# Optimization experiments

Measured on AMD Instinct MI355X. Metric: run time of the kernel, lower is better.

The kernel has to match this reference:

```python
import jax, jax.numpy as jnp
import numpy as np

MARGIN = 0.1
SCALE_POS = 2.0
SCALE_NEG = 50.0
THRESH = 0.5
EPS = 1e-5


def setup_inputs() -> dict:
    key = jax.random.key(0)
    k1, k2 = jax.random.split(key)
    feats = jax.random.normal(k1, (4096, 2, 192), dtype=jnp.float32)
    labels = jax.random.randint(k2, (4096,), 0, 4096, dtype=jnp.int64)
    return {"feats": feats, "labels": labels}


def reference(feats, labels):
    B, n_utt, D = feats.shape
    lab = jnp.repeat(labels, n_utt)            # [N]
    f = feats.reshape(-1, D)                   # [N, D]
    N = f.shape[0]

    sim = f @ f.T                              # [N, N]
    # F.normalize(sim): L2-normalize each row, eps=1e-12
    row_norm = jnp.maximum(jnp.linalg.norm(sim, axis=1, keepdims=True), 1e-12)
    S = sim / row_norm

    same = lab[None, :] == lab[:, None]        # [N, N]
    pos_mask = same & (S < 1.0 - EPS)          # pos_pair_ (includes self if < 1-eps)
    neg_mask = ~same                           # neg_pair_

    min_pos = jnp.min(jnp.where(pos_mask, S, jnp.inf), axis=1)    # per-row min(pos_pair_)
    max_neg = jnp.max(jnp.where(neg_mask, S, -jnp.inf), axis=1)   # per-row max(neg_pair_)

    neg_keep = neg_mask & (S > (min_pos - MARGIN)[:, None])
    pos_keep = pos_mask & (S < (max_neg + MARGIN)[:, None])

    has_neg = jnp.any(neg_keep, axis=1)
    has_pos = jnp.any(pos_keep, axis=1)
    valid = has_neg & has_pos

    pos_sum = jnp.sum(jnp.where(pos_keep, jnp.exp(-SCALE_POS * (S - THRESH)), 0.0), axis=1)
    neg_sum = jnp.sum(jnp.where(neg_keep, jnp.exp(SCALE_NEG * (S - THRESH)), 0.0), axis=1)

    row_loss = (1.0 / SCALE_POS) * jnp.log1p(pos_sum) + (1.0 / SCALE_NEG) * jnp.log1p(neg_sum)
    loss = jnp.sum(jnp.where(valid, row_loss, 0.0)) / N

    # prec1 = percent of rows skipped for having no surviving negatives
    prec1 = jnp.sum(~has_neg).astype(jnp.float32) * 100.0 / N
    return loss, prec1
```

## Files before the change

kernel.cpp:

```cpp
#include <hip/hip_runtime.h>
#include <math.h>

typedef float  f32x4  __attribute__((ext_vector_type(4)));
typedef int    int4v  __attribute__((ext_vector_type(4)));
typedef int    int8v  __attribute__((ext_vector_type(8)));

constexpr float MARGIN    = 0.1f;
constexpr float SCALE_POS = 2.0f;
constexpr float SCALE_NEG = 50.0f;
constexpr float THRESH    = 0.5f;
constexpr float ONE_EPS   = 1.0f - 1e-5f;
constexpr float LOG2E     = 1.4426950408889634f;
constexpr float BC        = -(SCALE_NEG * THRESH * LOG2E);
constexpr float VCUT_COEF = (36.0674f - 30.0f) / (SCALE_NEG * LOG2E);

constexpr int D      = 192;
constexpr int KP     = 256;
constexpr int RT     = 4;
constexpr int RPW    = 64;
constexpr int RPB    = 256;
constexpr int CSPLIT = 32;

constexpr int TILE_B8 = 4096;
constexpr int SCALE1  = 0x7f7f7f7f;

__device__ inline float fast_exp2(float x) {
#if __has_builtin(__builtin_amdgcn_exp2f)
  return __builtin_amdgcn_exp2f(x);
#else
  return exp2f(x);
#endif
}

__device__ inline void pin_frag8(int8v& v) {
  asm volatile("" : "+v"(v));
}

__global__ __launch_bounds__(1024) void k_prep(
    const float* __restrict__ f, unsigned char* __restrict__ pk8, int nrows,
    const int* __restrict__ labs, int* __restrict__ hist_g, int* __restrict__ offs_g,
    int* __restrict__ bucket, float* __restrict__ accum, int n)
{
  if (blockIdx.x < 64) {
    int gid = blockIdx.x * 1024 + threadIdx.x;
    int r = gid >> 3, j = gid & 7;
    if (r >= nrows) return;
    float x[32];
    if (j < 6) {
      const float* src = f + (size_t)r * D + j * 32;
#pragma unroll
      for (int i = 0; i < 8; ++i) {
        float4 v = *(const float4*)(src + i * 4);
        x[i * 4 + 0] = v.x; x[i * 4 + 1] = v.y; x[i * 4 + 2] = v.z; x[i * 4 + 3] = v.w;
      }
    } else {
#pragma unroll
      for (int i = 0; i < 32; ++i) x[i] = 0.f;
    }
    union { int s[8]; int8v v; } u;
#pragma unroll
    for (int i = 0; i < 8; ++i) {
      int p = __builtin_amdgcn_cvt_pk_fp8_f32(x[i * 4 + 0], x[i * 4 + 1], 0, false);
      p     = __builtin_amdgcn_cvt_pk_fp8_f32(x[i * 4 + 2], x[i * 4 + 3], p, true);
      u.s[i] = p;
    }
    int tile = r >> 4, c = r & 15, g = j >> 2, qq = j & 3;
    *(int8v*)(pk8 + (size_t)tile * TILE_B8 + g * 2048 + (qq * 16 + c) * 32) = u.v;
    return;
  }

  __shared__ int histL[4096];
  __shared__ int offsL[4096];
  __shared__ int scanb[1024];
  const int t = threadIdx.x;

  if (t < 3) accum[t] = 0.f;
  for (int i = t; i < 4096; i += 1024) histL[i] = 0;
  __syncthreads();
  for (int i = t; i < n; i += 1024) atomicAdd(&histL[labs[i]], 1);
  __syncthreads();
  int base = t * 4;
  int v[4]; int ls = 0;
  for (int k = 0; k < 4; ++k) { v[k] = ls; ls += histL[base + k]; }
  scanb[t] = ls;
  __syncthreads();
  for (int o = 1; o < 1024; o <<= 1) {
    int x = (t >= o) ? scanb[t - o] : 0;
    __syncthreads();
    scanb[t] += x;
    __syncthreads();
  }
  int ebase = scanb[t] - ls;
  for (int k = 0; k < 4; ++k) {
    offsL[base + k] = ebase + v[k];
    offs_g[base + k] = ebase + v[k];
    hist_g[base + k] = histL[base + k];
  }
  __syncthreads();
  for (int i = t; i < 4096; i += 1024) histL[i] = 0;
  __syncthreads();
  for (int i = t; i < n; i += 1024) {
    int lab = labs[i];
    int p = atomicAdd(&histL[lab], 1);
    bucket[offsL[lab] + p] = i;
  }
}

__global__ __launch_bounds__(256, 2) void k_pass1(
    const unsigned char* __restrict__ pk8, const int* __restrict__ labs,
    float* __restrict__ sumsqP, float* __restrict__ maxnegP,
    int N, int cps)
{
  __shared__ int ldsLab[512];

  const int tid  = threadIdx.x;
  const int lane = tid & 63;
  const int w    = tid >> 6;
  const int q    = lane >> 4;
  const int c    = lane & 15;
  const int cs   = blockIdx.x & (CSPLIT - 1);
  const int rbb  = blockIdx.x / CSPLIT;
  const int rowbase = rbb * RPB + w * RPW;
  const int col0 = cs * cps;
  const int ctile0 = col0 >> 4;
  const int ntiles = cps >> 4;

  for (int i = tid; i < cps; i += 256) ldsLab[i] = labs[(col0 + i) >> 1];

  int8v afr[RT][2];
#pragma unroll
  for (int rt = 0; rt < RT; ++rt)
#pragma unroll
    for (int g = 0; g < 2; ++g) {
      afr[rt][g] = *(const int8v*)(pk8 + (size_t)((rowbase >> 4) + rt) * TILE_B8 + g * 2048 + lane * 32);
      pin_frag8(afr[rt][g]);
    }

  int labrow[RT][4];
#pragma unroll
  for (int rt = 0; rt < RT; ++rt)
#pragma unroll
    for (int rr = 0; rr < 4; ++rr)
      labrow[rt][rr] = labs[(rowbase + rt * 16 + q * 4 + rr) >> 1];

  float ssq[RT][4], mxn[RT][4];
#pragma unroll
  for (int rt = 0; rt < RT; ++rt)
#pragma unroll
    for (int rr = 0; rr < 4; ++rr) { ssq[rt][rr] = 0.f; mxn[rt][rr] = -INFINITY; }

  __syncthreads();

  auto loadB = [&](int tile, int8v (&bf)[2]) {
    const unsigned char* bp = pk8 + (size_t)(ctile0 + tile) * TILE_B8 + lane * 32;
#pragma unroll
    for (int g = 0; g < 2; ++g) bf[g] = *(const int8v*)(bp + g * 2048);
  };
  auto compute = [&](const int8v (&bf)[2], int t) {
    const int labcol = ldsLab[t * 16 + c];
    f32x4 acc[RT];
#pragma unroll
    for (int rt = 0; rt < RT; ++rt) acc[rt] = 0.f;
#pragma unroll
    for (int g = 0; g < 2; ++g)
#pragma unroll
      for (int rt = 0; rt < RT; ++rt)
        acc[rt] = __builtin_amdgcn_mfma_scale_f32_16x16x128_f8f6f4(
            afr[rt][g], bf[g], acc[rt], 0, 0, 0, SCALE1, 0, SCALE1);
#pragma unroll
    for (int rt = 0; rt < RT; ++rt)
#pragma unroll
      for (int rr = 0; rr < 4; ++rr) {
        float v = acc[rt][rr];
        ssq[rt][rr] = fmaf(v, v, ssq[rt][rr]);
        float vm = (labrow[rt][rr] == labcol) ? -INFINITY : v;
        mxn[rt][rr] = fmaxf(mxn[rt][rr], vm);
      }
  };

  auto wrap = [&](int x) { return (x < ntiles) ? x : 0; };
  int8v b0[2], b1[2], b2[2], b3[2];
  loadB(0, b0);
  loadB(1, b1);
  for (int t = 0; t < ntiles; t += 4) {
    loadB(wrap(t + 2), b2); compute(b0, t);
    loadB(wrap(t + 3), b3); compute(b1, t + 1);
    loadB(wrap(t + 4), b0); compute(b2, t + 2);
    loadB(wrap(t + 5), b1); compute(b3, t + 3);
  }

#pragma unroll
  for (int rt = 0; rt < RT; ++rt)
#pragma unroll
    for (int rr = 0; rr < 4; ++rr) {
      float s = ssq[rt][rr], m = mxn[rt][rr];
#pragma unroll
      for (int msk = 1; msk < 16; msk <<= 1) {
        s += __shfl_xor(s, msk, 64);
        m = fmaxf(m, __shfl_xor(m, msk, 64));
      }
      if (c == 0) {
        int row = rowbase + rt * 16 + q * 4 + rr;
        sumsqP[(size_t)cs * N + row] = s;
        maxnegP[(size_t)cs * N + row] = m;
      }
    }
}

__global__ void k_rowstats(
    const float* __restrict__ f, const int* __restrict__ labs,
    const float* __restrict__ sumsqP, const float* __restrict__ maxnegP,
    const int* __restrict__ offs, const int* __restrict__ hist, const int* __restrict__ bucket,
    float* __restrict__ nthr2, float* __restrict__ arow,
    float* __restrict__ validf, float* __restrict__ hasnegf, float* __restrict__ posloss,
    int N)
{
  const int lane = threadIdx.x & 63;
  const int row  = blockIdx.x * 4 + (threadIdx.x >> 6);

  float s = 0.f, m = -INFINITY;
  if (lane < CSPLIT) {
    s = sumsqP[(size_t)lane * N + row];
    m = maxnegP[(size_t)lane * N + row];
  }
#pragma unroll
  for (int msk = 1; msk < 64; msk <<= 1) {
    s += __shfl_xor(s, msk, 64);
    m = fmaxf(m, __shfl_xor(m, msk, 64));
  }
  float nrm = fmaxf(sqrtf(s), 1e-12f);
  float inv = 1.0f / nrm;
  float maxnegS = m * inv;
  float posth = fminf(ONE_EPS, maxnegS + MARGIN);

  const int lab = labs[row >> 1];
  const int beg = offs[lab], cnt = hist[lab];
  const float* fi = f + (size_t)row * D;
  float x0 = fi[lane], x1 = fi[lane + 64], x2 = fi[lane + 128];

  float minp = INFINITY, psum = 0.f; int pcnt = 0;
  for (int t = 0; t < cnt; ++t) {
    int smp = bucket[beg + t];
#pragma unroll
    for (int u = 0; u < 2; ++u) {
      const float* fj = f + (size_t)(smp * 2 + u) * D;
      float p = x0 * fj[lane] + x1 * fj[lane + 64] + x2 * fj[lane + 128];
#pragma unroll
      for (int msk = 1; msk < 64; msk <<= 1) p += __shfl_xor(p, msk, 64);
      minp = fminf(minp, p);
      float S = p * inv;
      if (S < posth) {
        psum += fast_exp2((THRESH - S) * (SCALE_POS * LOG2E));
        pcnt++;
      }
    }
  }

  float minS = minp * inv;
  float min_pos = (minS < ONE_EPS) ? minS : INFINITY;
  bool hneg = maxnegS > (min_pos - MARGIN);
  bool valid = hneg && (pcnt > 0);
  if (lane == 0) {
    nthr2[row]   = fmaxf((min_pos - MARGIN) * nrm, VCUT_COEF * nrm);
    arow[row]    = inv * (SCALE_NEG * LOG2E);
    validf[row]  = valid ? 1.f : 0.f;
    hasnegf[row] = hneg ? 1.f : 0.f;
    posloss[row] = valid ? ((1.0f / SCALE_POS) * log1pf(psum)) : 0.f;
  }
}

__global__ __launch_bounds__(256, 2) void k_pass2(
    const unsigned char* __restrict__ pk8,
    const float* __restrict__ nthr2, const float* __restrict__ arow,
    const float* __restrict__ maxnegP,
    float* __restrict__ negsumP, int N, int cps)
{
  const int lane = threadIdx.x & 63;
  const int w    = threadIdx.x >> 6;
  const int q    = lane >> 4;
  const int c    = lane & 15;
  const int cs   = blockIdx.x & (CSPLIT - 1);
  const int rbb  = blockIdx.x / CSPLIT;
  const int rowbase = rbb * RPB + w * RPW;
  const int ctile0 = (cs * cps) >> 4;
  const int ntiles = cps >> 4;

  {
    int myrow = rowbase + lane;
    float mn = maxnegP[(size_t)cs * N + myrow];
    float th = nthr2[myrow];
    unsigned long long bal = __ballot(mn > th);
    if (bal == 0ull) {
      negsumP[(size_t)cs * N + myrow] = 0.f;
      return;
    }
  }

  int8v afr[RT][2];
#pragma unroll
  for (int rt = 0; rt < RT; ++rt)
#pragma unroll
    for (int g = 0; g < 2; ++g) {
      afr[rt][g] = *(const int8v*)(pk8 + (size_t)((rowbase >> 4) + rt) * TILE_B8 + g * 2048 + lane * 32);
      pin_frag8(afr[rt][g]);
    }

  float nthrv[RT][4], arw[RT][4], ns[RT][4];
#pragma unroll
  for (int rt = 0; rt < RT; ++rt)
#pragma unroll
    for (int rr = 0; rr < 4; ++rr) {
      int row = rowbase + rt * 16 + q * 4 + rr;
      nthrv[rt][rr] = nthr2[row];
      arw[rt][rr]   = arow[row];
      ns[rt][rr]    = 0.f;
    }

  auto loadB = [&](int tile, int8v (&bf)[2]) {
    const unsigned char* bp = pk8 + (size_t)(ctile0 + tile) * TILE_B8 + lane * 32;
#pragma unroll
    for (int g = 0; g < 2; ++g) bf[g] = *(const int8v*)(bp + g * 2048);
  };
  auto compute = [&](const int8v (&bf)[2]) {
    f32x4 acc[RT];
#pragma unroll
    for (int rt = 0; rt < RT; ++rt) acc[rt] = 0.f;
#pragma unroll
    for (int g = 0; g < 2; ++g)
#pragma unroll
      for (int rt = 0; rt < RT; ++rt)
        acc[rt] = __builtin_amdgcn_mfma_scale_f32_16x16x128_f8f6f4(
            afr[rt][g], bf[g], acc[rt], 0, 0, 0, SCALE1, 0, SCALE1);
#pragma unroll
    for (int rt = 0; rt < RT; ++rt)
#pragma unroll
      for (int rr = 0; rr < 4; ++rr) {
        float v = acc[rt][rr];
        float e = fast_exp2(fmaf(v, arw[rt][rr], BC));
        ns[rt][rr] += (v > nthrv[rt][rr]) ? e : 0.f;
      }
  };

  int8v b0[2], b1[2];
  loadB(0, b0);
  for (int t = 0; t < ntiles; t += 2) {
    loadB(t + 1, b1);
    compute(b0);
    int nx = t + 2; nx = (nx < ntiles) ? nx : 0;
    loadB(nx, b0);
    compute(b1);
  }

#pragma unroll
  for (int rt = 0; rt < RT; ++rt)
#pragma unroll
    for (int rr = 0; rr < 4; ++rr) {
      float sv = ns[rt][rr];
#pragma unroll
      for (int msk = 1; msk < 16; msk <<= 1) sv += __shfl_xor(sv, msk, 64);
      if (c == 0) {
        int row = rowbase + rt * 16 + q * 4 + rr;
        negsumP[(size_t)cs * N + row] = sv;
      }
    }
}

__global__ void k_final(const float* __restrict__ negsumP, const float* __restrict__ posloss,
                        const float* __restrict__ validf, const float* __restrict__ hasnegf,
                        float* __restrict__ accum, float* __restrict__ out, int N)
{
  int i = blockIdx.x * blockDim.x + threadIdx.x;
  float lacc = 0.f, nacc = 0.f;
  if (i < N) {
    float nsum = 0.f;
    for (int cs2 = 0; cs2 < CSPLIT; ++cs2) nsum += negsumP[(size_t)cs2 * N + i];
    lacc = validf[i] * (posloss[i] + (1.0f / SCALE_NEG) * log1pf(nsum));
    nacc = 1.0f - hasnegf[i];
  }
#pragma unroll
  for (int msk = 1; msk < 64; msk <<= 1) {
    lacc += __shfl_xor(lacc, msk, 64);
    nacc += __shfl_xor(nacc, msk, 64);
  }
  __shared__ float sl[4], sn[4];
  __shared__ bool isLast;
  int wid = threadIdx.x >> 6, lane = threadIdx.x & 63;
  if (lane == 0) { sl[wid] = lacc; sn[wid] = nacc; }
  __syncthreads();
  if (threadIdx.x == 0) {
    float L = sl[0] + sl[1] + sl[2] + sl[3];
    float Nn = sn[0] + sn[1] + sn[2] + sn[3];
    atomicAdd(&accum[0], L);
    atomicAdd(&accum[1], Nn);
    __threadfence();
    int tkt = atomicAdd((int*)&accum[2], 1);
    isLast = (tkt == (int)gridDim.x - 1);
  }
  __syncthreads();
  if (isLast && threadIdx.x == 0) {
    __threadfence();
    out[0] = accum[0] / (float)N;
    out[1] = accum[1] * 100.0f / (float)N;
  }
}

extern "C" void kernel_launch(void* const* d_in, const int* in_sizes, int n_in,
                              void* d_out, int out_size, void* d_ws, size_t ws_size,
                              hipStream_t stream)
{
  (void)n_in; (void)out_size; (void)ws_size;
  const float* f    = (const float*)d_in[0];
  const int*   labs = (const int*)d_in[1];
  const int Bs = in_sizes[1];
  const int N  = 2 * Bs;

  char* ws = (char*)d_ws;
  size_t off = 0;
  auto alloc = [&](size_t bytes) -> void* {
    void* p = ws + off;
    off += (bytes + 255) & ~(size_t)255;
    return p;
  };
  unsigned char* pk8 = (unsigned char*)alloc((size_t)N * KP);
  float* sumsqP  = (float*)alloc((size_t)CSPLIT * N * sizeof(float));
  float* maxnegP = (float*)alloc((size_t)CSPLIT * N * sizeof(float));
  float* negsumP = (float*)alloc((size_t)CSPLIT * N * sizeof(float));
  float* nthr2   = (float*)alloc((size_t)N * sizeof(float));
  float* arow    = (float*)alloc((size_t)N * sizeof(float));
  float* validf  = (float*)alloc((size_t)N * sizeof(float));
  float* hasnegf = (float*)alloc((size_t)N * sizeof(float));
  float* posloss = (float*)alloc((size_t)N * sizeof(float));
  int* hist   = (int*)alloc((size_t)Bs * sizeof(int));
  int* offs   = (int*)alloc((size_t)Bs * sizeof(int));
  int* bucket = (int*)alloc((size_t)Bs * sizeof(int));
  float* accum = (float*)alloc(4 * sizeof(float));

  k_prep<<<65, 1024, 0, stream>>>(f, pk8, N, labs, hist, offs, bucket, accum, Bs);

  const int cps   = N / CSPLIT;
  const int grid1 = (N / RPB) * CSPLIT;
  k_pass1<<<grid1, 256, 0, stream>>>(pk8, labs, sumsqP, maxnegP, N, cps);
  k_rowstats<<<N / 4, 256, 0, stream>>>(f, labs, sumsqP, maxnegP, offs, hist, bucket,
                                        nthr2, arow, validf, hasnegf, posloss, N);
  k_pass2<<<grid1, 256, 0, stream>>>(pk8, nthr2, arow, maxnegP, negsumP, N, cps);
  k_final<<<N / 256, 256, 0, stream>>>(negsumP, posloss, validf, hasnegf, accum, (float*)d_out, N);
}
```

Before: 109.4 us.

## Use single-wave blocks for both pass kernels and drop LDS label staging

```diff
diff --git a/kernel.cpp b/kernel.cpp
--- a/kernel.cpp
+++ b/kernel.cpp
@@ -2,7 +2,6 @@
 #include <math.h>
 
 typedef float  f32x4  __attribute__((ext_vector_type(4)));
-typedef int    int4v  __attribute__((ext_vector_type(4)));
 typedef int    int8v  __attribute__((ext_vector_type(8)));
 
 constexpr float MARGIN    = 0.1f;
@@ -18,7 +17,6 @@
 constexpr int KP     = 256;
 constexpr int RT     = 4;
 constexpr int RPW    = 64;
-constexpr int RPB    = 256;
 constexpr int CSPLIT = 32;
 
 constexpr int TILE_B8 = 4096;
@@ -106,27 +104,21 @@
   }
 }
 
-__global__ __launch_bounds__(256, 2) void k_pass1(
+__global__ __launch_bounds__(64) void k_pass1(
     const unsigned char* __restrict__ pk8, const int* __restrict__ labs,
     float* __restrict__ sumsqP, float* __restrict__ maxnegP,
     int N, int cps)
 {
-  __shared__ int ldsLab[512];
-
-  const int tid  = threadIdx.x;
-  const int lane = tid & 63;
-  const int w    = tid >> 6;
+  const int lane = threadIdx.x;
   const int q    = lane >> 4;
   const int c    = lane & 15;
   const int cs   = blockIdx.x & (CSPLIT - 1);
-  const int rbb  = blockIdx.x / CSPLIT;
-  const int rowbase = rbb * RPB + w * RPW;
+  const int rb   = blockIdx.x / CSPLIT;
+  const int rowbase = rb * RPW;
   const int col0 = cs * cps;
   const int ctile0 = col0 >> 4;
   const int ntiles = cps >> 4;
 
-  for (int i = tid; i < cps; i += 256) ldsLab[i] = labs[(col0 + i) >> 1];
-
   int8v afr[RT][2];
 #pragma unroll
   for (int rt = 0; rt < RT; ++rt)
@@ -149,15 +141,15 @@
 #pragma unroll
     for (int rr = 0; rr < 4; ++rr) { ssq[rt][rr] = 0.f; mxn[rt][rr] = -INFINITY; }
 
-  __syncthreads();
-
   auto loadB = [&](int tile, int8v (&bf)[2]) {
     const unsigned char* bp = pk8 + (size_t)(ctile0 + tile) * TILE_B8 + lane * 32;
 #pragma unroll
     for (int g = 0; g < 2; ++g) bf[g] = *(const int8v*)(bp + g * 2048);
   };
-  auto compute = [&](const int8v (&bf)[2], int t) {
-    const int labcol = ldsLab[t * 16 + c];
+  auto loadLab = [&](int tile) -> int {
+    return labs[(col0 + tile * 16 + c) >> 1];
+  };
+  auto compute = [&](const int8v (&bf)[2], int labcol) {
     f32x4 acc[RT];
 #pragma unroll
     for (int rt = 0; rt < RT; ++rt) acc[rt] = 0.f;
@@ -178,15 +170,17 @@
       }
   };
 
-  auto wrap = [&](int x) { return (x < ntiles) ? x : 0; };
-  int8v b0[2], b1[2], b2[2], b3[2];
+  int8v b0[2], b1[2];
+  int lc0 = loadLab(0), lc1;
   loadB(0, b0);
-  loadB(1, b1);
-  for (int t = 0; t < ntiles; t += 4) {
-    loadB(wrap(t + 2), b2); compute(b0, t);
-    loadB(wrap(t + 3), b3); compute(b1, t + 1);
-    loadB(wrap(t + 4), b0); compute(b2, t + 2);
-    loadB(wrap(t + 5), b1); compute(b3, t + 3);
+  for (int t = 0; t < ntiles; t += 2) {
+    loadB(t + 1, b1);
+    lc1 = loadLab(t + 1);
+    compute(b0, lc0);
+    int nx = t + 2; nx = (nx < ntiles) ? nx : 0;
+    loadB(nx, b0);
+    lc0 = loadLab(nx);
+    compute(b1, lc1);
   }
 
 #pragma unroll
@@ -269,19 +263,18 @@
   }
 }
 
-__global__ __launch_bounds__(256, 2) void k_pass2(
+__global__ __launch_bounds__(64) void k_pass2(
     const unsigned char* __restrict__ pk8,
     const float* __restrict__ nthr2, const float* __restrict__ arow,
     const float* __restrict__ maxnegP,
     float* __restrict__ negsumP, int N, int cps)
 {
-  const int lane = threadIdx.x & 63;
-  const int w    = threadIdx.x >> 6;
+  const int lane = threadIdx.x;
   const int q    = lane >> 4;
   const int c    = lane & 15;
   const int cs   = blockIdx.x & (CSPLIT - 1);
-  const int rbb  = blockIdx.x / CSPLIT;
-  const int rowbase = rbb * RPB + w * RPW;
+  const int rb   = blockIdx.x / CSPLIT;
+  const int rowbase = rb * RPW;
   const int ctile0 = (cs * cps) >> 4;
   const int ntiles = cps >> 4;
 
@@ -438,10 +431,10 @@
   k_prep<<<65, 1024, 0, stream>>>(f, pk8, N, labs, hist, offs, bucket, accum, Bs);
 
   const int cps   = N / CSPLIT;
-  const int grid1 = (N / RPB) * CSPLIT;
-  k_pass1<<<grid1, 256, 0, stream>>>(pk8, labs, sumsqP, maxnegP, N, cps);
+  const int grid1 = (N / RPW) * CSPLIT;
+  k_pass1<<<grid1, 64, 0, stream>>>(pk8, labs, sumsqP, maxnegP, N, cps);
   k_rowstats<<<N / 4, 256, 0, stream>>>(f, labs, sumsqP, maxnegP, offs, hist, bucket,
                                         nthr2, arow, validf, hasnegf, posloss, N);
-  k_pass2<<<grid1, 256, 0, stream>>>(pk8, nthr2, arow, maxnegP, negsumP, N, cps);
+  k_pass2<<<grid1, 64, 0, stream>>>(pk8, nthr2, arow, maxnegP, negsumP, N, cps);
   k_final<<<N / 256, 256, 0, stream>>>(negsumP, posloss, validf, hasnegf, accum, (float*)d_out, N);
 }
```

Result: slower. 114.9 us (+5.1%).
